# Kernel tuning notes

Hardware: AMD Instinct MI355X
Metric: run time of the kernel (lower is better)

## Reference

```python
import jax, jax.numpy as jnp
import numpy as np

N, E, B = 30000, 300000, 64
F_N, F_E, F_G, H = 64, 32, 32, 64
EPS = 1e-5


def _bn(t, gamma, beta):
    # BatchNorm1d in training mode: biased batch statistics over the row dim.
    m = t.mean(axis=0)
    v = t.var(axis=0)
    return gamma * (t - m) * jax.lax.rsqrt(v + EPS) + beta


def _seg_mean(vals, idx, num):
    s = jax.ops.segment_sum(vals, idx, num_segments=num)
    c = jax.ops.segment_sum(jnp.ones((vals.shape[0], 1), vals.dtype), idx,
                            num_segments=num)
    return s / jnp.maximum(c, 1.0)


def setup_inputs() -> dict:
    key = jax.random.key(0)
    ks = jax.random.split(key, 32)
    inp = {
        'x': jax.random.normal(ks[0], (N, F_N), jnp.float32),
        'edge_index': jax.random.randint(ks[1], (2, E), 0, N),
        'e': jax.random.normal(ks[2], (E, F_E), jnp.float32),
        'u': jax.random.normal(ks[3], (B, F_G), jnp.float32),
        'batch': jnp.sort(jax.random.randint(ks[4], (N,), 0, B)),
        'g_node': jnp.ones((F_N,), jnp.float32),
        'b_node': jnp.zeros((F_N,), jnp.float32),
        'g_edge': jnp.ones((F_E,), jnp.float32),
        'b_edge': jnp.zeros((F_E,), jnp.float32),
        'g_glob': jnp.ones((F_G,), jnp.float32),
        'b_glob': jnp.zeros((F_G,), jnp.float32),
    }
    # Per-step Linear weights; input dims follow the feature-size threading in __init__.
    din_e = [2 * F_N + F_E + F_G, 3 * H + H, 3 * H + H]  # [192, 256, 256]
    din_n = [F_N + H + F_G, H + H + H, H + H + H]        # [160, 192, 192]
    din_g = [H + F_G, H + H, H + H]                      # [96, 128, 128]
    k = 5
    for l in range(3):
        for tag, din in (('e', din_e[l]), ('n', din_n[l]), ('g', din_g[l])):
            inp[f'W{tag}{l}'] = jax.random.normal(ks[k], (din, H), jnp.float32) / np.sqrt(din)
            inp[f'b{tag}{l}'] = jnp.zeros((H,), jnp.float32)
            k += 1
    return inp


def _forward(x, e, u, batch, src, dst,
             g_node, b_node, g_edge, b_edge, g_glob, b_glob,
             We, be, Wn, bn, Wg, bg):
    # Input normalization
    x = _bn(x, g_node, b_node)
    e = _bn(e, g_edge, b_edge)
    u = _bn(u, g_glob, b_glob)
    for l in range(3):
        # Edge model: per-edge MLP over [x_src, x_dst, e, u_edge]
        e_in = jnp.concatenate([x[src], x[dst], e, u[batch[src]]], axis=-1)
        e = jax.nn.relu(e_in @ We[l] + be[l])
        # Node model: aggregate incoming messages at destination (mean)
        agg = _seg_mean(e, dst, N)
        n_in = jnp.concatenate([x, agg, u[batch]], axis=-1)
        x = jax.nn.relu(n_in @ Wn[l] + bn[l])
        # Global model: mean-pool nodes per graph
        g_in = jnp.concatenate([_seg_mean(x, batch, B), u], axis=-1)
        u = jax.nn.relu(g_in @ Wg[l] + bg[l])
    return x, e, u


def reference(x, edge_index, e, u, batch,
              g_node, b_node, g_edge, b_edge, g_glob, b_glob,
              We0, be0, Wn0, bn0, Wg0, bg0,
              We1, be1, Wn1, bn1, Wg1, bg1,
              We2, be2, Wn2, bn2, Wg2, bg2):
    src, dst = edge_index[0], edge_index[1]
    We = (We0, We1, We2); be = (be0, be1, be2)
    Wn = (Wn0, Wn1, Wn2); bn = (bn0, bn1, bn2)
    Wg = (Wg0, Wg1, Wg2); bg = (bg0, bg1, bg2)
    return _forward(x, e, u, batch, src, dst,
                    g_node, b_node, g_edge, b_edge, g_glob, b_glob,
                    We, be, Wn, bn, Wg, bg)
```

## Files before the change

### kernel.cpp

```cpp
#include <hip/hip_runtime.h>
#include <hip/hip_bf16.h>

#define EPS 1e-5f
typedef __hip_bfloat16 bf16;
typedef __attribute__((ext_vector_type(8))) short  short8;
typedef __attribute__((ext_vector_type(4))) float  f32x4;

__device__ __forceinline__ float b2f(bf16 v) { return __bfloat162float(v); }
__device__ __forceinline__ float bs2f(short s) { bf16 b = *reinterpret_cast<bf16*>(&s); return b2f(b); }
__device__ __forceinline__ float ldv(const void* p, size_t i, bool bf) {
    return bf ? b2f(((const bf16*)p)[i]) : ((const float*)p)[i];
}
__device__ __forceinline__ void stv(void* p, size_t i, float v, bool bf) {
    if (bf) ((bf16*)p)[i] = __float2bfloat16(v);
    else    ((float*)p)[i] = v;
}
__device__ __forceinline__ short f2bs(float v) {
    bf16 b = __float2bfloat16(v);
    return *reinterpret_cast<short*>(&b);
}
__device__ __forceinline__ short8 ld16s(const short* p) { return *(const short8*)p; }

__global__ void detect_dtype(const unsigned short* __restrict__ xs, float* __restrict__ flag) {
    __shared__ int cnt;
    if (threadIdx.x == 0) cnt = 0;
    __syncthreads();
    unsigned short u = xs[threadIdx.x];
    int e = (u >> 7) & 0xFF;
    int sane = (u == 0 || (e >= 110 && e <= 140)) ? 1 : 0;
    atomicAdd(&cnt, sane);
    __syncthreads();
    if (threadIdx.x == 0) flag[0] = (cnt >= 230) ? 1.0f : 0.0f;
}

template<int C>
__global__ __launch_bounds__(256) void bn_stats(const void* __restrict__ in, int R,
                                                float* __restrict__ stats, const float* __restrict__ flag) {
    bool isbf = flag[0] != 0.f;
    const int RG = 256 / C;
    int c = threadIdx.x % C, rg = threadIdx.x / C;
    float s = 0.f, s2 = 0.f;
    if (isbf) {
        const bf16* ip = (const bf16*)in;
        for (int r = blockIdx.x * RG + rg; r < R; r += gridDim.x * RG) {
            float v = b2f(ip[(size_t)r * C + c]); s += v; s2 += v * v;
        }
    } else {
        const float* ip = (const float*)in;
        for (int r = blockIdx.x * RG + rg; r < R; r += gridDim.x * RG) {
            float v = ip[(size_t)r * C + c]; s += v; s2 += v * v;
        }
    }
    __shared__ float sm[2][256];
    sm[0][threadIdx.x] = s; sm[1][threadIdx.x] = s2;
    __syncthreads();
    if (threadIdx.x < C) {
        float ts = 0.f, t2 = 0.f;
        for (int g = 0; g < RG; g++) { ts += sm[0][g * C + c]; t2 += sm[1][g * C + c]; }
        atomicAdd(&stats[c], ts);
        atomicAdd(&stats[C + c], t2);
    }
}

__global__ __launch_bounds__(256) void bn_apply_x(const void* __restrict__ in, short* __restrict__ out,
                                                  const float* __restrict__ stats, int R,
                                                  const void* __restrict__ gamma, const void* __restrict__ beta,
                                                  const float* __restrict__ flag) {
    bool isbf = flag[0] != 0.f;
    int total = R * 64;
    for (int i = blockIdx.x * 256 + threadIdx.x; i < total; i += gridDim.x * 256) {
        int c = i & 63;
        float mean = stats[c] / (float)R;
        float var = stats[64 + c] / (float)R - mean * mean;
        float inv = rsqrtf(var + EPS);
        out[i] = f2bs(ldv(gamma, c, isbf) * (ldv(in, i, isbf) - mean) * inv + ldv(beta, c, isbf));
    }
}

__global__ __launch_bounds__(256) void bn_apply_u(const void* __restrict__ in, float* __restrict__ outf,
                                                  short* __restrict__ outb,
                                                  const float* __restrict__ stats, int R,
                                                  const void* __restrict__ gamma, const void* __restrict__ beta,
                                                  const float* __restrict__ flag) {
    bool isbf = flag[0] != 0.f;
    int total = R * 32;
    for (int i = blockIdx.x * 256 + threadIdx.x; i < total; i += gridDim.x * 256) {
        int c = i & 31;
        float mean = stats[c] / (float)R;
        float var = stats[32 + c] / (float)R - mean * mean;
        float inv = rsqrtf(var + EPS);
        float v = ldv(gamma, c, isbf) * (ldv(in, i, isbf) - mean) * inv + ldv(beta, c, isbf);
        outf[i] = v; outb[i] = f2bs(v);
    }
}

__global__ __launch_bounds__(256) void count_kernel(const int* __restrict__ ei, int* __restrict__ cnt, int E) {
    int stride = gridDim.x * 256;
    for (int t = blockIdx.x * 256 + threadIdx.x; t < E; t += stride) atomicAdd(&cnt[ei[E + t]], 1);
}

__global__ __launch_bounds__(256) void csr_offsets(const int* __restrict__ cnt, int* __restrict__ off,
                                                   int* __restrict__ wcur, int* __restrict__ cursor, int N,
                                                   const int* __restrict__ batch, int* __restrict__ gstart, int B) {
    int n = blockIdx.x * 256 + threadIdx.x;
    if (n < N) {
        int o = atomicAdd(cursor, cnt[n]);
        off[n] = o; wcur[n] = o;
    }
    if (blockIdx.x == 0 && threadIdx.x <= B) {
        int t = threadIdx.x;
        int lo = 0, hi = N;
        while (lo < hi) { int mid = (lo + hi) >> 1; if (batch[mid] < t) lo = mid + 1; else hi = mid; }
        gstart[t] = lo;
    }
}

__global__ __launch_bounds__(256) void csr_fill(const int* __restrict__ ei, int* __restrict__ wcur,
                                                int* __restrict__ csr, int E) {
    int stride = gridDim.x * 256;
    for (int t = blockIdx.x * 256 + threadIdx.x; t < E; t += stride) {
        int d = ei[E + t];
        int pos = atomicAdd(&wcur[d], 1);
        csr[pos] = t;
    }
}

__global__ __launch_bounds__(256) void perm_build(const int* __restrict__ ei, const int* __restrict__ csr,
                                                  int* __restrict__ sp, int* __restrict__ dp, int E) {
    int stride = gridDim.x * 256;
    for (int t = blockIdx.x * 256 + threadIdx.x; t < E; t += stride) {
        int e0 = csr[t];
        sp[t] = ei[e0];
        dp[t] = ei[E + e0];
    }
}

__global__ __launch_bounds__(256) void transpose_w(
    const void* __restrict__ W0, const void* __restrict__ W1, const void* __restrict__ W2,
    const void* __restrict__ W3, const void* __restrict__ W4, const void* __restrict__ W5,
    short* __restrict__ out, const float* __restrict__ flag)
{
    bool isbf = flag[0] != 0.f;
    const void* Ws[6] = {W0, W1, W2, W3, W4, W5};
    const int   din[6] = {192, 256, 256, 160, 192, 192};
    int mtx = blockIdx.x >> 3;
    int off = 0;
    for (int i = 0; i < mtx; i++) off += 64 * din[i];
    int d = din[mtx];
    const void* W = Ws[mtx];
    for (int i = (blockIdx.x & 7) * 256 + threadIdx.x; i < 64 * d; i += 8 * 256) {
        int n = i / d, k = i % d;
        out[off + n * d + k] = f2bs(ldv(W, (size_t)k * 64 + n, isbf));
    }
}

template<bool L0>
__global__ __launch_bounds__(256) void edge_mfma(
    const int* __restrict__ sp, const int* __restrict__ dp,
    const int* __restrict__ csrv,
    const int* __restrict__ batchv,
    const short* __restrict__ xb,
    const void* __restrict__ ein, size_t ein_off,
    const float* __restrict__ estats, const void* __restrict__ egamma, const void* __restrict__ ebeta,
    const short* __restrict__ ub,
    const short* __restrict__ Wt, const void* __restrict__ biasv,
    void* __restrict__ eout, size_t eout_off,
    int E, const float* __restrict__ flag,
    int ein_force_bf, int eout_force_bf, int eout_orig, short* __restrict__ eout2)
{
    constexpr int DIN = L0 ? 192 : 256;
    constexpr int NQ = DIN / 32;
    constexpr int ROWB = DIN * 2;
    __shared__ __align__(16) char Wl[64 * ROWB];
    __shared__ __align__(16) char T[4 * 2048];
    const bool isbf = flag[0] != 0.f;
    const bool ein_bf = ein_force_bf ? true : isbf;
    const bool eout_bf = eout_force_bf ? true : isbf;
    const int w = threadIdx.x >> 6, j = threadIdx.x & 63;
    const int m16 = j & 15, c8v = j >> 4, c8 = c8v * 8;
    const int rr8 = j >> 3, cc8 = j & 7;

    for (int i = threadIdx.x; i < DIN * 8; i += 256) {
        int lin = i * 16;
        int row = i / (DIN / 8);
        *(short8*)(Wl + (lin ^ ((row & 7) << 4))) = *(const short8*)(Wt + i * 8);
    }
    __syncthreads();

    char* Tw = T + w * 2048;
    const int wkey = (m16 & 7) << 4;

    float sc[8], sh[8];
    if constexpr (L0) {
        #pragma unroll
        for (int k = 0; k < 8; k++) {
            int col = c8 + k;
            float m = estats[col] / (float)E;
            float iv = rsqrtf(estats[32 + col] / (float)E - m * m + EPS);
            sc[k] = ldv(egamma, col, isbf) * iv;
            sh[k] = ldv(ebeta, col, isbf) - m * sc[k];
        }
    }
    float bc[4];
    #pragma unroll
    for (int t = 0; t < 4; t++) bc[t] = ldv(biasv, t * 16 + m16, isbf);

    const int ntiles = (E + 63) >> 6;
    const int gs = gridDim.x;
    int tile = blockIdx.x;
    if (tile < ntiles) {
        int ec = tile * 64 + w * 16 + m16; if (ec > E - 1) ec = E - 1;
        int s = sp[ec], d = dp[ec];
        int eo = ec;
        if constexpr (L0) { if (csrv) eo = csrv[ec]; }
        for (; tile < ntiles; tile += gs) {
            const int ecC = ec, sC = s, dC = d, eoC = eo;
            const int tn = tile + gs;
            if (tn < ntiles) {
                int e2 = tn * 64 + w * 16 + m16; if (e2 > E - 1) e2 = E - 1;
                ec = e2; s = sp[e2]; d = dp[e2];
                if constexpr (L0) { if (csrv) eo = csrv[e2]; }
            }
            int g = batchv[sC];

            short8 af[NQ];
            af[0] = ld16s(xb + (size_t)sC * 64 + c8);
            af[1] = ld16s(xb + (size_t)sC * 64 + 32 + c8);
            af[2] = ld16s(xb + (size_t)dC * 64 + c8);
            af[3] = ld16s(xb + (size_t)dC * 64 + 32 + c8);
            if constexpr (L0) {
                float ev[8];
                if (isbf) {
                    short8 r = ld16s((const short*)ein + (size_t)eoC * 32 + c8);
                    #pragma unroll
                    for (int k = 0; k < 8; k++) ev[k] = bs2f(r[k]);
                } else {
                    const float* ef = (const float*)ein + (size_t)eoC * 32 + c8;
                    float4 a = *(const float4*)ef, b = *(const float4*)(ef + 4);
                    ev[0]=a.x; ev[1]=a.y; ev[2]=a.z; ev[3]=a.w; ev[4]=b.x; ev[5]=b.y; ev[6]=b.z; ev[7]=b.w;
                }
                #pragma unroll
                for (int k = 0; k < 8; k++) af[4][k] = f2bs(ev[k] * sc[k] + sh[k]);
                af[5] = ld16s(ub + (size_t)g * 32 + c8);
            } else {
                if (ein_bf) {
                    af[4] = ld16s((const short*)ein + ein_off + (size_t)ecC * 64 + c8);
                    af[5] = ld16s((const short*)ein + ein_off + (size_t)ecC * 64 + 32 + c8);
                } else {
                    const float* ef = (const float*)ein + ein_off + (size_t)ecC * 64;
                    float4 a = *(const float4*)(ef + c8), b = *(const float4*)(ef + c8 + 4);
                    af[4][0]=f2bs(a.x); af[4][1]=f2bs(a.y); af[4][2]=f2bs(a.z); af[4][3]=f2bs(a.w);
                    af[4][4]=f2bs(b.x); af[4][5]=f2bs(b.y); af[4][6]=f2bs(b.z); af[4][7]=f2bs(b.w);
                    a = *(const float4*)(ef + 32 + c8); b = *(const float4*)(ef + 36 + c8);
                    af[5][0]=f2bs(a.x); af[5][1]=f2bs(a.y); af[5][2]=f2bs(a.z); af[5][3]=f2bs(a.w);
                    af[5][4]=f2bs(b.x); af[5][5]=f2bs(b.y); af[5][6]=f2bs(b.z); af[5][7]=f2bs(b.w);
                }
                af[6] = ld16s(ub + (size_t)g * 64 + c8);
                af[7] = ld16s(ub + (size_t)g * 64 + 32 + c8);
            }

            f32x4 acc[4] = {{0,0,0,0},{0,0,0,0},{0,0,0,0},{0,0,0,0}};
            #pragma unroll
            for (int q = 0; q < NQ; q++) {
                #pragma unroll
                for (int t = 0; t < 4; t++) {
                    int lin = (t * 16 + m16) * ROWB + q * 64 + c8v * 16;
                    short8 bv = *(const short8*)(Wl + (lin ^ wkey));
                    acc[t] = __builtin_amdgcn_mfma_f32_16x16x32_bf16(af[q], bv, acc[t], 0, 0, 0);
                }
            }

            const int we = tile * 64 + w * 16;
            #pragma unroll
            for (int t = 0; t < 4; t++) {
                #pragma unroll
                for (int r = 0; r < 4; r++) {
                    float v = fmaxf(acc[t][r] + bc[t], 0.f);
                    int rr = c8v * 4 + r;
                    int lin = rr * 128 + (t * 16 + m16) * 2;
                    *(short*)(Tw + (lin ^ ((rr & 7) << 4))) = f2bs(v);
                }
            }
            #pragma unroll
            for (int i = 0; i < 2; i++) {
                int r = i * 8 + rr8;
                int e2 = we + r;
                if (e2 < E) {
                    short8 row = *(const short8*)(Tw + ((r * 128 + cc8 * 16) ^ ((rr8 & 7) << 4)));
                    int rowIdx = (eout_orig && csrv) ? csrv[e2] : e2;
                    if (eout_bf) {
                        *(short8*)((short*)eout + eout_off + (size_t)rowIdx * 64 + cc8 * 8) = row;
                    } else {
                        float* op = (float*)eout + eout_off + (size_t)rowIdx * 64 + cc8 * 8;
                        float4 a, b;
                        a.x=bs2f(row[0]); a.y=bs2f(row[1]); a.z=bs2f(row[2]); a.w=bs2f(row[3]);
                        b.x=bs2f(row[4]); b.y=bs2f(row[5]); b.z=bs2f(row[6]); b.w=bs2f(row[7]);
                        *(float4*)op = a; *(float4*)(op + 4) = b;
                    }
                    if (eout2) {
                        *(short8*)(eout2 + (size_t)e2 * 64 + cc8 * 8) = row;
                    }
                }
            }
        }
    }
}

template<bool L0, bool FINAL>
__global__ __launch_bounds__(256) void node_fused(
    const int* __restrict__ batchv, const short* __restrict__ xin,
    const int* __restrict__ off, const int* __restrict__ csr, const int* __restrict__ cntv,
    const void* __restrict__ eout, size_t eoff,
    const short* __restrict__ ub,
    const short* __restrict__ Wt, const void* __restrict__ biasv,
    short* __restrict__ xoutb, void* __restrict__ dout, int N,
    const float* __restrict__ flag, int e_force_bf, int contig)
{
    constexpr int DIN = L0 ? 160 : 192;
    constexpr int NQ = DIN / 32;
    constexpr int ROWB = DIN * 2;
    __shared__ __align__(16) char Wl[64 * ROWB];
    __shared__ __align__(16) char T[4 * 2048];
    const bool isbf = flag[0] != 0.f;
    const bool e_bf = e_force_bf ? true : isbf;
    const int w = threadIdx.x >> 6, j = threadIdx.x & 63;
    const int m16 = j & 15, c8v = j >> 4, c8 = c8v * 8;
    const int rr8 = j >> 3, cc8 = j & 7;
    const int nb = blockIdx.x * 64 + w * 16;

    for (int i = threadIdx.x; i < DIN * 8; i += 256) {
        int lin = i * 16;
        int row = i / (DIN / 8);
        *(short8*)(Wl + (lin ^ ((row & 7) << 4))) = *(const short8*)(Wt + i * 8);
    }
    __syncthreads();

    char* Tw = T + w * 2048;
    const int wkey = (m16 & 7) << 4;

    int n = nb + m16; if (n > N - 1) n = N - 1;
    int g = batchv[n];

    short8 af[NQ];
    af[0] = ld16s(xin + (size_t)n * 64 + c8);
    af[1] = ld16s(xin + (size_t)n * 64 + 32 + c8);

    {
        int st = off[n], c = cntv[n];
        float s0[8] = {0,0,0,0,0,0,0,0}, s1[8] = {0,0,0,0,0,0,0,0};
        if (e_bf) {
            const short* ep = (const short*)eout + eoff;
            if (contig) {
                const short* base = ep + (size_t)st * 64;
                int t = 0;
                for (; t + 2 <= c; t += 2) {
                    short8 r0 = ld16s(base + (size_t)t * 64 + c8);
                    short8 q0 = ld16s(base + (size_t)t * 64 + 32 + c8);
                    short8 r1 = ld16s(base + (size_t)(t + 1) * 64 + c8);
                    short8 q1 = ld16s(base + (size_t)(t + 1) * 64 + 32 + c8);
                    #pragma unroll
                    for (int k = 0; k < 8; k++) { s0[k] += bs2f(r0[k]) + bs2f(r1[k]); s1[k] += bs2f(q0[k]) + bs2f(q1[k]); }
                }
                if (t < c) {
                    short8 r0 = ld16s(base + (size_t)t * 64 + c8);
                    short8 q0 = ld16s(base + (size_t)t * 64 + 32 + c8);
                    #pragma unroll
                    for (int k = 0; k < 8; k++) { s0[k] += bs2f(r0[k]); s1[k] += bs2f(q0[k]); }
                }
            } else {
                int t = 0;
                for (; t + 2 <= c; t += 2) {
                    int e0 = csr[st + t], e1 = csr[st + t + 1];
                    short8 r0 = ld16s(ep + (size_t)e0 * 64 + c8);
                    short8 q0 = ld16s(ep + (size_t)e0 * 64 + 32 + c8);
                    short8 r1 = ld16s(ep + (size_t)e1 * 64 + c8);
                    short8 q1 = ld16s(ep + (size_t)e1 * 64 + 32 + c8);
                    #pragma unroll
                    for (int k = 0; k < 8; k++) { s0[k] += bs2f(r0[k]) + bs2f(r1[k]); s1[k] += bs2f(q0[k]) + bs2f(q1[k]); }
                }
                if (t < c) {
                    int e0 = csr[st + t];
                    short8 r0 = ld16s(ep + (size_t)e0 * 64 + c8);
                    short8 q0 = ld16s(ep + (size_t)e0 * 64 + 32 + c8);
                    #pragma unroll
                    for (int k = 0; k < 8; k++) { s0[k] += bs2f(r0[k]); s1[k] += bs2f(q0[k]); }
                }
            }
        } else {
            const float* ep = (const float*)eout + eoff;
            for (int t = 0; t < c; t++) {
                int e0 = csr[st + t];
                const float* rp = ep + (size_t)e0 * 64;
                float4 a = *(const float4*)(rp + c8), b = *(const float4*)(rp + c8 + 4);
                float4 x = *(const float4*)(rp + 32 + c8), y = *(const float4*)(rp + 36 + c8);
                s0[0]+=a.x; s0[1]+=a.y; s0[2]+=a.z; s0[3]+=a.w; s0[4]+=b.x; s0[5]+=b.y; s0[6]+=b.z; s0[7]+=b.w;
                s1[0]+=x.x; s1[1]+=x.y; s1[2]+=x.z; s1[3]+=x.w; s1[4]+=y.x; s1[5]+=y.y; s1[6]+=y.z; s1[7]+=y.w;
            }
        }
        float rc = 1.0f / fmaxf((float)c, 1.0f);
        #pragma unroll
        for (int k = 0; k < 8; k++) { af[2][k] = f2bs(s0[k] * rc); af[3][k] = f2bs(s1[k] * rc); }
    }

    if constexpr (L0) {
        af[4] = ld16s(ub + (size_t)g * 32 + c8);
    } else {
        af[4] = ld16s(ub + (size_t)g * 64 + c8);
        af[5] = ld16s(ub + (size_t)g * 64 + 32 + c8);
    }

    f32x4 acc[4] = {{0,0,0,0},{0,0,0,0},{0,0,0,0},{0,0,0,0}};
    #pragma unroll
    for (int q = 0; q < NQ; q++) {
        #pragma unroll
        for (int t = 0; t < 4; t++) {
            int lin = (t * 16 + m16) * ROWB + q * 64 + c8v * 16;
            short8 bv = *(const short8*)(Wl + (lin ^ wkey));
            acc[t] = __builtin_amdgcn_mfma_f32_16x16x32_bf16(af[q], bv, acc[t], 0, 0, 0);
        }
    }

    #pragma unroll
    for (int t = 0; t < 4; t++) {
        float bcv = ldv(biasv, t * 16 + m16, isbf);
        #pragma unroll
        for (int r = 0; r < 4; r++) {
            float v = fmaxf(acc[t][r] + bcv, 0.f);
            int rr = c8v * 4 + r;
            int lin = rr * 128 + (t * 16 + m16) * 2;
            *(short*)(Tw + (lin ^ ((rr & 7) << 4))) = f2bs(v);
        }
    }
    #pragma unroll
    for (int i = 0; i < 2; i++) {
        int r = i * 8 + rr8;
        int n2 = nb + r;
        if (n2 < N) {
            short8 row = *(const short8*)(Tw + ((r * 128 + cc8 * 16) ^ ((rr8 & 7) << 4)));
            *(short8*)&xoutb[(size_t)n2 * 64 + cc8 * 8] = row;
            if (FINAL) {
                if (isbf) {
                    *(short8*)((short*)dout + (size_t)n2 * 64 + cc8 * 8) = row;
                } else {
                    float* op = (float*)dout + (size_t)n2 * 64 + cc8 * 8;
                    float4 a, b;
                    a.x=bs2f(row[0]); a.y=bs2f(row[1]); a.z=bs2f(row[2]); a.w=bs2f(row[3]);
                    b.x=bs2f(row[4]); b.y=bs2f(row[5]); b.z=bs2f(row[6]); b.w=bs2f(row[7]);
                    *(float4*)op = a; *(float4*)(op + 4) = b;
                }
            }
        }
    }
}

__global__ __launch_bounds__(256) void pool_kernel(const int* __restrict__ gstart,
                                                   const short* __restrict__ xb,
                                                   float* __restrict__ gsum) {
    int g = blockIdx.x >> 3, slice = blockIdx.x & 7;
    int st = gstart[g], en = gstart[g + 1];
    int len = en - st;
    int K = (len + 7) >> 3;
    int b0 = st + slice * K;
    int b1 = min(b0 + K, en);
    int rg = threadIdx.x >> 3, cc8 = threadIdx.x & 7;
    float a[8] = {0,0,0,0,0,0,0,0};
    for (int r = b0 + rg; r < b1; r += 32) {
        short8 v = *(const short8*)&xb[(size_t)r * 64 + cc8 * 8];
        #pragma unroll
        for (int k = 0; k < 8; k++) a[k] += bs2f(v[k]);
    }
    __shared__ float sm[32][64];
    #pragma unroll
    for (int k = 0; k < 8; k++) sm[rg][cc8 * 8 + k] = a[k];
    __syncthreads();
    if (threadIdx.x < 64) {
        float s = 0.f;
        #pragma unroll 8
        for (int q = 0; q < 32; q++) s += sm[q][threadIdx.x];
        atomicAdd(&gsum[g * 64 + threadIdx.x], s);
    }
}

template<int FU>
__global__ __launch_bounds__(256) void glob_gemm(
    const int* __restrict__ gstart, const float* __restrict__ gsum,
    const float* __restrict__ uin,
    const void* __restrict__ W, const void* __restrict__ biasv,
    float* __restrict__ uoutf, short* __restrict__ uoutb,
    const float* __restrict__ flag)
{
    bool isbf = flag[0] != 0.f;
    const int DIN = 64 + FU;
    __shared__ float s[4][192];
    int w = threadIdx.x >> 6, j = threadIdx.x & 63;
    int g = blockIdx.x * 4 + w;
    int st = gstart[g], en = gstart[g + 1];
    float rc = 1.0f / fmaxf((float)(en - st), 1.0f);
    s[w][j] = gsum[g * 64 + j] * rc;
    if (j < FU) s[w][64 + j] = uin[g * FU + j];
    float acc = ldv(biasv, j, isbf);
    for (int k = 0; k < DIN; k++) acc += s[w][k] * ldv(W, (size_t)k * 64 + j, isbf);
    acc = fmaxf(acc, 0.f);
    uoutf[g * 64 + j] = acc;
    uoutb[g * 64 + j] = f2bs(acc);
}

__global__ __launch_bounds__(256) void cast_out(const float* __restrict__ in, void* __restrict__ out,
                                                size_t out_off, int n, const float* __restrict__ flag) {
    bool isbf = flag[0] != 0.f;
    for (int i = blockIdx.x * 256 + threadIdx.x; i < n; i += gridDim.x * 256)
        stv(out, out_off + i, in[i], isbf);
}

extern "C" void kernel_launch(void* const* d_in, const int* in_sizes, int n_in,
                              void* d_out, int out_size, void* d_ws, size_t ws_size,
                              hipStream_t stream) {
    const void* x_in   = d_in[0];
    const int*  ei     = (const int*)d_in[1];
    const void* e_raw  = d_in[2];
    const void* u_raw  = d_in[3];
    const int*  batchv = (const int*)d_in[4];
    const void *g_node = d_in[5],  *b_node = d_in[6];
    const void *g_edge = d_in[7],  *b_edge = d_in[8];
    const void *g_glob = d_in[9],  *b_glob = d_in[10];
    const void* We[3] = {d_in[11], d_in[17], d_in[23]};
    const void* be[3] = {d_in[12], d_in[18], d_in[24]};
    const void* Wn[3] = {d_in[13], d_in[19], d_in[25]};
    const void* bn[3] = {d_in[14], d_in[20], d_in[26]};
    const void* Wg[3] = {d_in[15], d_in[21], d_in[27]};
    const void* bg[3] = {d_in[16], d_in[22], d_in[28]};

    const int N = in_sizes[0] / 64;
    const int E = in_sizes[2] / 32;
    const int B = in_sizes[3] / 32;

    float* p = (float*)d_ws;
    float* zbase  = p;
    float* stats  = p; p += 3 * 128;
    int*   cursor = (int*)p; p += 4;
    int*   cnt    = (int*)p; p += N;
    float* gsum0  = p; p += B * 64;
    float* gsum1  = p; p += B * 64;
    float* gsum2  = p; p += B * 64;
    size_t zbytes = (size_t)((char*)p - (char*)zbase);
    float* dflag  = p; p += 4;
    float* uN     = p; p += B * 32;
    float* uA     = p; p += B * 64;
    float* uB     = p; p += B * 64;
    int*   off    = (int*)p; p += N;
    int*   wcur   = (int*)p; p += N;
    int*   gstart = (int*)p; p += 72;
    int*   csr    = (int*)p; p += E;
    int*   sp     = (int*)p; p += E;
    int*   dp     = (int*)p; p += E;
    short* xb0    = (short*)p; p += (size_t)N * 32;
    short* xb1    = (short*)p; p += (size_t)N * 32;
    short* ubN    = (short*)p; p += B * 16;
    short* ubA    = (short*)p; p += B * 32;
    short* ubB    = (short*)p; p += B * 32;
    short* WtAll  = (short*)p; p += 79872 / 2;
    const short* WtE0 = WtAll;
    const short* WtE1 = WtAll + 12288;
    const short* WtE2 = WtAll + 28672;
    const short* WtN0 = WtAll + 45056;
    const short* WtN1 = WtAll + 55296;
    const short* WtN2 = WtAll + 67584;

    short* eb16 = nullptr;
    {
        size_t used = (size_t)((char*)p - (char*)d_ws);
        used = (used + 15) & ~(size_t)15;
        size_t need = used + (size_t)E * 64 * sizeof(short);
        if (ws_size >= need) eb16 = (short*)((char*)d_ws + used);
    }

    const size_t EOFF = (size_t)N * 64;
    const size_t UOFF = EOFF + (size_t)E * 64;

    hipMemsetAsync(zbase, 0, zbytes, stream);

    detect_dtype<<<1, 256, 0, stream>>>((const unsigned short*)x_in, dflag);

    bn_stats<64><<<256, 256, 0, stream>>>(x_in, N, stats, dflag);
    bn_stats<32><<<512, 256, 0, stream>>>(e_raw, E, stats + 128, dflag);
    bn_stats<32><<<8,   256, 0, stream>>>(u_raw, B, stats + 256, dflag);
    bn_apply_x<<<512, 256, 0, stream>>>(x_in, xb0, stats, N, g_node, b_node, dflag);
    bn_apply_u<<<8,   256, 0, stream>>>(u_raw, uN, ubN, stats + 256, B, g_glob, b_glob, dflag);
    count_kernel<<<512, 256, 0, stream>>>(ei, cnt, E);
    csr_offsets<<<(N + 255) / 256, 256, 0, stream>>>(cnt, off, wcur, cursor, N, batchv, gstart, B);
    csr_fill<<<512, 256, 0, stream>>>(ei, wcur, csr, E);
    perm_build<<<512, 256, 0, stream>>>(ei, csr, sp, dp, E);
    transpose_w<<<48, 256, 0, stream>>>(We[0], We[1], We[2], Wn[0], Wn[1], Wn[2], WtAll, dflag);

    const int NG = (N + 63) / 64;
    const int NT = (E + 63) / 64;
    const int EG0 = NT < 1280 ? NT : 1280;
    const int EG  = NT < 1024 ? NT : 1024;

    if (eb16) {
        edge_mfma<true><<<EG0, 256, 0, stream>>>(
            sp, dp, csr, batchv, xb0, e_raw, 0, stats + 128, g_edge, b_edge,
            ubN, WtE0, be[0], eb16, 0, E, dflag, 0, 1, 0, nullptr);
        node_fused<true, false><<<NG, 256, 0, stream>>>(
            batchv, xb0, off, csr, cnt, eb16, 0, ubN, WtN0, bn[0], xb1, nullptr, N, dflag, 1, 1);
        pool_kernel<<<B * 8, 256, 0, stream>>>(gstart, xb1, gsum0);
        glob_gemm<32><<<B / 4, 256, 0, stream>>>(gstart, gsum0, uN, Wg[0], bg[0], uA, ubA, dflag);

        edge_mfma<false><<<EG, 256, 0, stream>>>(
            sp, dp, csr, batchv, xb1, eb16, 0, nullptr, nullptr, nullptr,
            ubA, WtE1, be[1], eb16, 0, E, dflag, 1, 1, 0, nullptr);
        node_fused<false, false><<<NG, 256, 0, stream>>>(
            batchv, xb1, off, csr, cnt, eb16, 0, ubA, WtN1, bn[1], xb0, nullptr, N, dflag, 1, 1);
        pool_kernel<<<B * 8, 256, 0, stream>>>(gstart, xb0, gsum1);
        glob_gemm<64><<<B / 4, 256, 0, stream>>>(gstart, gsum1, uA, Wg[1], bg[1], uB, ubB, dflag);

        edge_mfma<false><<<EG, 256, 0, stream>>>(
            sp, dp, csr, batchv, xb0, eb16, 0, nullptr, nullptr, nullptr,
            ubB, WtE2, be[2], d_out, EOFF, E, dflag, 1, 0, 1, eb16);
        node_fused<false, true><<<NG, 256, 0, stream>>>(
            batchv, xb0, off, csr, cnt, eb16, 0, ubB, WtN2, bn[2], xb1, d_out, N, dflag, 1, 1);
        pool_kernel<<<B * 8, 256, 0, stream>>>(gstart, xb1, gsum2);
        glob_gemm<64><<<B / 4, 256, 0, stream>>>(gstart, gsum2, uB, Wg[2], bg[2], uA, ubA, dflag);
    } else {
        edge_mfma<true><<<EG0, 256, 0, stream>>>(
            ei, ei + E, nullptr, batchv, xb0, e_raw, 0, stats + 128, g_edge, b_edge,
            ubN, WtE0, be[0], d_out, EOFF, E, dflag, 0, 0, 0, nullptr);
        node_fused<true, false><<<NG, 256, 0, stream>>>(
            batchv, xb0, off, csr, cnt, d_out, EOFF, ubN, WtN0, bn[0], xb1, nullptr, N, dflag, 0, 0);
        pool_kernel<<<B * 8, 256, 0, stream>>>(gstart, xb1, gsum0);
        glob_gemm<32><<<B / 4, 256, 0, stream>>>(gstart, gsum0, uN, Wg[0], bg[0], uA, ubA, dflag);

        edge_mfma<false><<<EG, 256, 0, stream>>>(
            ei, ei + E, nullptr, batchv, xb1, d_out, EOFF, nullptr, nullptr, nullptr,
            ubA, WtE1, be[1], d_out, EOFF, E, dflag, 0, 0, 0, nullptr);
        node_fused<false, false><<<NG, 256, 0, stream>>>(
            batchv, xb1, off, csr, cnt, d_out, EOFF, ubA, WtN1, bn[1], xb0, nullptr, N, dflag, 0, 0);
        pool_kernel<<<B * 8, 256, 0, stream>>>(gstart, xb0, gsum1);
        glob_gemm<64><<<B / 4, 256, 0, stream>>>(gstart, gsum1, uA, Wg[1], bg[1], uB, ubB, dflag);

        edge_mfma<false><<<EG, 256, 0, stream>>>(
            ei, ei + E, nullptr, batchv, xb0, d_out, EOFF, nullptr, nullptr, nullptr,
            ubB, WtE2, be[2], d_out, EOFF, E, dflag, 0, 0, 0, nullptr);
        node_fused<false, true><<<NG, 256, 0, stream>>>(
            batchv, xb0, off, csr, cnt, d_out, EOFF, ubB, WtN2, bn[2], xb1, d_out, N, dflag, 0, 0);
        pool_kernel<<<B * 8, 256, 0, stream>>>(gstart, xb1, gsum2);
        glob_gemm<64><<<B / 4, 256, 0, stream>>>(gstart, gsum2, uB, Wg[2], bg[2], uA, ubA, dflag);
    }

    cast_out<<<16, 256, 0, stream>>>(uA, d_out, UOFF, B * 64, dflag);
}
```

Baseline: 472.0 us.

## Fuse global pooling into node kernel and drop extra launches

Graph-level mean pooling moves into the node kernel epilogue. When a 16-row wave tile lies in one graph, its rows are reduced in registers and with shuffles before one atomic per column; otherwise it falls back to per-element atomics. The separate perm_build pass is folded into csr_fill, and the final cast kernel is replaced by glob_gemm writing straight to the output. This removes several launches and a re-read of node features, at the cost of more float atomics whose summation order is nondeterministic.

```diff
diff --git a/kernel.cpp b/kernel.cpp
--- a/kernel.cpp
+++ b/kernel.cpp
@@ -116,22 +116,15 @@
 }
 
 __global__ __launch_bounds__(256) void csr_fill(const int* __restrict__ ei, int* __restrict__ wcur,
-                                                int* __restrict__ csr, int E) {
+                                                int* __restrict__ csr, int* __restrict__ sp,
+                                                int* __restrict__ dp, int E) {
     int stride = gridDim.x * 256;
     for (int t = blockIdx.x * 256 + threadIdx.x; t < E; t += stride) {
-        int d = ei[E + t];
+        int s = ei[t], d = ei[E + t];
         int pos = atomicAdd(&wcur[d], 1);
         csr[pos] = t;
-    }
-}
-
-__global__ __launch_bounds__(256) void perm_build(const int* __restrict__ ei, const int* __restrict__ csr,
-                                                  int* __restrict__ sp, int* __restrict__ dp, int E) {
-    int stride = gridDim.x * 256;
-    for (int t = blockIdx.x * 256 + threadIdx.x; t < E; t += stride) {
-        int e0 = csr[t];
-        sp[t] = ei[e0];
-        dp[t] = ei[E + e0];
+        sp[pos] = s;
+        dp[pos] = d;
     }
 }
 
@@ -314,7 +307,8 @@
     const short* __restrict__ ub,
     const short* __restrict__ Wt, const void* __restrict__ biasv,
     short* __restrict__ xoutb, void* __restrict__ dout, int N,
-    const float* __restrict__ flag, int e_force_bf, int contig)
+    const float* __restrict__ flag, int e_force_bf, int contig,
+    float* __restrict__ gsum)
 {
     constexpr int DIN = L0 ? 160 : 192;
     constexpr int NQ = DIN / 32;
@@ -388,8 +382,9 @@
             }
         } else {
             const float* ep = (const float*)eout + eoff;
-            for (int t = 0; t < c; t++) {
-                int e0 = csr[st + t];
+            int st2 = st, c2 = cntv[n];
+            for (int t = 0; t < c2; t++) {
+                int e0 = csr[st2 + t];
                 const float* rp = ep + (size_t)e0 * 64;
                 float4 a = *(const float4*)(rp + c8), b = *(const float4*)(rp + c8 + 4);
                 float4 x = *(const float4*)(rp + 32 + c8), y = *(const float4*)(rp + 36 + c8);
@@ -431,6 +426,10 @@
             *(short*)(Tw + (lin ^ ((rr & 7) << 4))) = f2bs(v);
         }
     }
+
+    const bool fast = (nb + 15 <= N - 1) && (batchv[nb] == batchv[nb + 15]);
+    float ps[8] = {0,0,0,0,0,0,0,0};
+
     #pragma unroll
     for (int i = 0; i < 2; i++) {
         int r = i * 8 + rr8;
@@ -449,35 +448,26 @@
                     *(float4*)op = a; *(float4*)(op + 4) = b;
                 }
             }
-        }
-    }
-}
-
-__global__ __launch_bounds__(256) void pool_kernel(const int* __restrict__ gstart,
-                                                   const short* __restrict__ xb,
-                                                   float* __restrict__ gsum) {
-    int g = blockIdx.x >> 3, slice = blockIdx.x & 7;
-    int st = gstart[g], en = gstart[g + 1];
-    int len = en - st;
-    int K = (len + 7) >> 3;
-    int b0 = st + slice * K;
-    int b1 = min(b0 + K, en);
-    int rg = threadIdx.x >> 3, cc8 = threadIdx.x & 7;
-    float a[8] = {0,0,0,0,0,0,0,0};
-    for (int r = b0 + rg; r < b1; r += 32) {
-        short8 v = *(const short8*)&xb[(size_t)r * 64 + cc8 * 8];
+            if (fast) {
+                #pragma unroll
+                for (int k = 0; k < 8; k++) ps[k] += bs2f(row[k]);
+            } else {
+                int g2 = batchv[n2];
+                #pragma unroll
+                for (int k = 0; k < 8; k++) atomicAdd(&gsum[g2 * 64 + cc8 * 8 + k], bs2f(row[k]));
+            }
+        }
+    }
+    if (fast) {
+        int gw = batchv[nb];
         #pragma unroll
-        for (int k = 0; k < 8; k++) a[k] += bs2f(v[k]);
-    }
-    __shared__ float sm[32][64];
-    #pragma unroll
-    for (int k = 0; k < 8; k++) sm[rg][cc8 * 8 + k] = a[k];
-    __syncthreads();
-    if (threadIdx.x < 64) {
-        float s = 0.f;
-        #pragma unroll 8
-        for (int q = 0; q < 32; q++) s += sm[q][threadIdx.x];
-        atomicAdd(&gsum[g * 64 + threadIdx.x], s);
+        for (int k = 0; k < 8; k++) {
+            float v = ps[k];
+            v += __shfl_xor(v, 8);
+            v += __shfl_xor(v, 16);
+            v += __shfl_xor(v, 32);
+            if (rr8 == 0) atomicAdd(&gsum[gw * 64 + cc8 * 8 + k], v);
+        }
     }
 }
 
@@ -487,7 +477,8 @@
     const float* __restrict__ uin,
     const void* __restrict__ W, const void* __restrict__ biasv,
     float* __restrict__ uoutf, short* __restrict__ uoutb,
-    const float* __restrict__ flag)
+    const float* __restrict__ flag,
+    void* __restrict__ dOut, size_t uoff, int writeD)
 {
     bool isbf = flag[0] != 0.f;
     const int DIN = 64 + FU;
@@ -501,15 +492,12 @@
     float acc = ldv(biasv, j, isbf);
     for (int k = 0; k < DIN; k++) acc += s[w][k] * ldv(W, (size_t)k * 64 + j, isbf);
     acc = fmaxf(acc, 0.f);
-    uoutf[g * 64 + j] = acc;
-    uoutb[g * 64 + j] = f2bs(acc);
-}
-
-__global__ __launch_bounds__(256) void cast_out(const float* __restrict__ in, void* __restrict__ out,
-                                                size_t out_off, int n, const float* __restrict__ flag) {
-    bool isbf = flag[0] != 0.f;
-    for (int i = blockIdx.x * 256 + threadIdx.x; i < n; i += gridDim.x * 256)
-        stv(out, out_off + i, in[i], isbf);
+    if (writeD) {
+        stv(dOut, uoff + (size_t)g * 64 + j, acc, isbf);
+    } else {
+        uoutf[g * 64 + j] = acc;
+        uoutb[g * 64 + j] = f2bs(acc);
+    }
 }
 
 extern "C" void kernel_launch(void* const* d_in, const int* in_sizes, int n_in,
@@ -588,8 +576,7 @@
     bn_apply_u<<<8,   256, 0, stream>>>(u_raw, uN, ubN, stats + 256, B, g_glob, b_glob, dflag);
     count_kernel<<<512, 256, 0, stream>>>(ei, cnt, E);
     csr_offsets<<<(N + 255) / 256, 256, 0, stream>>>(cnt, off, wcur, cursor, N, batchv, gstart, B);
-    csr_fill<<<512, 256, 0, stream>>>(ei, wcur, csr, E);
-    perm_build<<<512, 256, 0, stream>>>(ei, csr, sp, dp, E);
+    csr_fill<<<512, 256, 0, stream>>>(ei, wcur, csr, sp, dp, E);
     transpose_w<<<48, 256, 0, stream>>>(We[0], We[1], We[2], Wn[0], Wn[1], Wn[2], WtAll, dflag);
 
     const int NG = (N + 63) / 64;
@@ -602,50 +589,48 @@
             sp, dp, csr, batchv, xb0, e_raw, 0, stats + 128, g_edge, b_edge,
             ubN, WtE0, be[0], eb16, 0, E, dflag, 0, 1, 0, nullptr);
         node_fused<true, false><<<NG, 256, 0, stream>>>(
-            batchv, xb0, off, csr, cnt, eb16, 0, ubN, WtN0, bn[0], xb1, nullptr, N, dflag, 1, 1);
-        pool_kernel<<<B * 8, 256, 0, stream>>>(gstart, xb1, gsum0);
-        glob_gemm<32><<<B / 4, 256, 0, stream>>>(gstart, gsum0, uN, Wg[0], bg[0], uA, ubA, dflag);
+            batchv, xb0, off, csr, cnt, eb16, 0, ubN, WtN0, bn[0], xb1, nullptr, N, dflag, 1, 1, gsum0);
+        glob_gemm<32><<<B / 4, 256, 0, stream>>>(gstart, gsum0, uN, Wg[0], bg[0], uA, ubA, dflag,
+                                                 nullptr, 0, 0);
 
         edge_mfma<false><<<EG, 256, 0, stream>>>(
             sp, dp, csr, batchv, xb1, eb16, 0, nullptr, nullptr, nullptr,
             ubA, WtE1, be[1], eb16, 0, E, dflag, 1, 1, 0, nullptr);
         node_fused<false, false><<<NG, 256, 0, stream>>>(
-            batchv, xb1, off, csr, cnt, eb16, 0, ubA, WtN1, bn[1], xb0, nullptr, N, dflag, 1, 1);
-        pool_kernel<<<B * 8, 256, 0, stream>>>(gstart, xb0, gsum1);
-        glob_gemm<64><<<B / 4, 256, 0, stream>>>(gstart, gsum1, uA, Wg[1], bg[1], uB, ubB, dflag);
+            batchv, xb1, off, csr, cnt, eb16, 0, ubA, WtN1, bn[1], xb0, nullptr, N, dflag, 1, 1, gsum1);
+        glob_gemm<64><<<B / 4, 256, 0, stream>>>(gstart, gsum1, uA, Wg[1], bg[1], uB, ubB, dflag,
+                                                 nullptr, 0, 0);
 
         edge_mfma<false><<<EG, 256, 0, stream>>>(
             sp, dp, csr, batchv, xb0, eb16, 0, nullptr, nullptr, nullptr,
             ubB, WtE2, be[2], d_out, EOFF, E, dflag, 1, 0, 1, eb16);
         node_fused<false, true><<<NG, 256, 0, stream>>>(
-            batchv, xb0, off, csr, cnt, eb16, 0, ubB, WtN2, bn[2], xb1, d_out, N, dflag, 1, 1);
-        pool_kernel<<<B * 8, 256, 0, stream>>>(gstart, xb1, gsum2);
-        glob_gemm<64><<<B / 4, 256, 0, stream>>>(gstart, gsum2, uB, Wg[2], bg[2], uA, ubA, dflag);
+            batchv, xb0, off, csr, cnt, eb16, 0, ubB, WtN2, bn[2], xb1, d_out, N, dflag, 1, 1, gsum2);
+        glob_gemm<64><<<B / 4, 256, 0, stream>>>(gstart, gsum2, uB, Wg[2], bg[2], uA, ubA, dflag,
+                                                 d_out, UOFF, 1);
     } else {
         edge_mfma<true><<<EG0, 256, 0, stream>>>(
             ei, ei + E, nullptr, batchv, xb0, e_raw, 0, stats + 128, g_edge, b_edge,
             ubN, WtE0, be[0], d_out, EOFF, E, dflag, 0, 0, 0, nullptr);
         node_fused<true, false><<<NG, 256, 0, stream>>>(
-            batchv, xb0, off, csr, cnt, d_out, EOFF, ubN, WtN0, bn[0], xb1, nullptr, N, dflag, 0, 0);
-        pool_kernel<<<B * 8, 256, 0, stream>>>(gstart, xb1, gsum0);
-        glob_gemm<32><<<B / 4, 256, 0, stream>>>(gstart, gsum0, uN, Wg[0], bg[0], uA, ubA, dflag);
+            batchv, xb0, off, csr, cnt, d_out, EOFF, ubN, WtN0, bn[0], xb1, nullptr, N, dflag, 0, 0, gsum0);
+        glob_gemm<32><<<B / 4, 256, 0, stream>>>(gstart, gsum0, uN, Wg[0], bg[0], uA, ubA, dflag,
+                                                 nullptr, 0, 0);
 
         edge_mfma<false><<<EG, 256, 0, stream>>>(
             ei, ei + E, nullptr, batchv, xb1, d_out, EOFF, nullptr, nullptr, nullptr,
             ubA, WtE1, be[1], d_out, EOFF, E, dflag, 0, 0, 0, nullptr);
         node_fused<false, false><<<NG, 256, 0, stream>>>(
-            batchv, xb1, off, csr, cnt, d_out, EOFF, ubA, WtN1, bn[1], xb0, nullptr, N, dflag, 0, 0);
-        pool_kernel<<<B * 8, 256, 0, stream>>>(gstart, xb0, gsum1);
-        glob_gemm<64><<<B / 4, 256, 0, stream>>>(gstart, gsum1, uA, Wg[1], bg[1], uB, ubB, dflag);
+            batchv, xb1, off, csr, cnt, d_out, EOFF, ubA, WtN1, bn[1], xb0, nullptr, N, dflag, 0, 0, gsum1);
+        glob_gemm<64><<<B / 4, 256, 0, stream>>>(gstart, gsum1, uA, Wg[1], bg[1], uB, ubB, dflag,
+                                                 nullptr, 0, 0);
 
         edge_mfma<false><<<EG, 256, 0, stream>>>(
             ei, ei + E, nullptr, batchv, xb0, d_out, EOFF, nullptr, nullptr, nullptr,
             ubB, WtE2, be[2], d_out, EOFF, E, dflag, 0, 0, 0, nullptr);
         node_fused<false, true><<<NG, 256, 0, stream>>>(
-            batchv, xb0, off, csr, cnt, d_out, EOFF, ubB, WtN2, bn[2], xb1, d_out, N, dflag, 0, 0);
-        pool_kernel<<<B * 8, 256, 0, stream>>>(gstart, xb1, gsum2);
-        glob_gemm<64><<<B / 4, 256, 0, stream>>>(gstart, gsum2, uB, Wg[2], bg[2], uA, ubA, dflag);
-    }
-
-    cast_out<<<16, 256, 0, stream>>>(uA, d_out, UOFF, B * 64, dflag);
-}
+            batchv, xb0, off, csr, cnt, d_out, EOFF, ubB, WtN2, bn[2], xb1, d_out, N, dflag, 0, 0, gsum2);
+        glob_gemm<64><<<B / 4, 256, 0, stream>>>(gstart, gsum2, uB, Wg[2], bg[2], uA, ubA, dflag,
+                                                 d_out, UOFF, 1);
+    }
+}
```

Measured after the change: 501.8 us. 1.06x slower.
